# Kernel optimization log

Measured on AMD Instinct MI355X. Metric: run time of the kernel, lower is better.

## Reference

```python
import jax, jax.numpy as jnp
import numpy as np

NBINS = 256
HMIN, HMAX = 0.0, 255.0

def _histc(x, nbins=NBINS, lo=HMIN, hi=HMAX):
    # Faithful torch.histc: bin width (hi-lo)/nbins; values outside [lo,hi] ignored;
    # values == hi fall into the last bin. Returns float counts.
    xf = x.reshape(-1)
    width = (hi - lo) / nbins
    idx = jnp.floor((xf - lo) / width).astype(jnp.int32)
    idx = jnp.minimum(idx, nbins - 1)            # x == hi -> last bin
    in_range = (xf >= lo) & (xf <= hi)
    idx = jnp.where(in_range, idx, nbins)        # out-of-range -> dropped bucket
    hist = jnp.zeros(nbins + 1, dtype=x.dtype).at[idx].add(1.0)
    return hist[:nbins]

def setup_inputs() -> dict:
    key = jax.random.key(0)
    # intensity image with values in [0, 255]
    x = jax.random.uniform(key, (8192, 4096), dtype=jnp.float32) * 255.0
    return {"batchsize": 16, "input": x}

def reference(batchsize, input):
    hist = _histc(input)                          # [256] float counts
    # Original loop recomputes the same histc each iter and does
    # count += hist[0] (scalar broadcast into all 256 slots).
    count = jnp.zeros(NBINS, dtype=hist.dtype) + jnp.asarray(batchsize, hist.dtype) * hist[0]
    return (hist, count)
```

## Files before the change

kernel.cpp:

```cpp
#include <hip/hip_runtime.h>

#define NBINS 256
#define BLOCK 64
#define NQUAD 64
#define CNT_DW (NQUAD * 64)
#define LDS_DW (CNT_DW + 64)
#define BIN_SCALE (256.0f / 255.0f)
#define CAP_F4 62

__global__ void zero_out(float* __restrict__ out) {
    const int i = blockIdx.x * blockDim.x + threadIdx.x;
    if (i < 2 * NBINS) out[i] = 0.0f;
}

__device__ __forceinline__ void classify(float v, int t, int& dw, unsigned& inc) {
    int idx = (int)(v * BIN_SCALE);
    idx = idx < 255 ? idx : 255;
    const bool ok = (v >= 0.0f) && (v <= 255.0f);
    const int d = ((((unsigned)idx) >> 2) << 6) + t;
    dw = ok ? d : (CNT_DW + t);
    inc = 1u << ((idx & 3) << 3);
}

__global__ __launch_bounds__(BLOCK) void hist_kernel(const float* __restrict__ x,
                                                     unsigned int* __restrict__ partial,
                                                     float* __restrict__ out,
                                                     int n, int G, int use_ws) {
    __shared__ unsigned int cnt[LDS_DW];
    const int t = threadIdx.x;

    for (int i = t; i < LDS_DW; i += BLOCK) cnt[i] = 0u;
    __syncthreads();

    const int n4 = n >> 2;
    const float4* __restrict__ x4 = (const float4*)x;
    const int stride = G * BLOCK;
    int i = blockIdx.x * BLOCK + t;

    if (i < n4) {
        float4 v = x4[i];
        for (;;) {
            const int ni = i + stride;
            const bool more = ni < n4;
            float4 nv;
            if (more) nv = x4[ni];

            int d0, d1, d2, d3; unsigned s0, s1, s2, s3;
            classify(v.x, t, d0, s0);
            classify(v.y, t, d1, s1);
            classify(v.z, t, d2, s2);
            classify(v.w, t, d3, s3);

            unsigned o0 = cnt[d0], o1 = cnt[d1], o2 = cnt[d2], o3 = cnt[d3];
            cnt[d0] = o0 + s0;
            cnt[d1] = o1 + s1 + (d1 == d0 ? s0 : 0u);
            cnt[d2] = o2 + s2 + (d2 == d0 ? s0 : 0u) + (d2 == d1 ? s1 : 0u);
            cnt[d3] = o3 + s3 + (d3 == d0 ? s0 : 0u) + (d3 == d1 ? s1 : 0u)
                              + (d3 == d2 ? s2 : 0u);

            if (!more) break;
            v = nv; i = ni;
        }
    }
    for (int j = (n4 << 2) + blockIdx.x * BLOCK + t; j < n; j += stride) {
        int dw; unsigned inc;
        classify(x[j], t, dw, inc);
        cnt[dw] += inc;
    }
    __syncthreads();

    unsigned accA = 0, accB = 0;
#pragma unroll 16
    for (int k = 0; k < 64; ++k) {
        unsigned u = cnt[(t << 6) + ((t + k) & 63)];
        accA += u & 0x00FF00FFu;
        accB += (u >> 8) & 0x00FF00FFu;
    }
    const unsigned b0 = accA & 0xFFFFu, b2 = accA >> 16;
    const unsigned b1 = accB & 0xFFFFu, b3 = accB >> 16;

    if (use_ws) {
        ((uint4*)(partial + (size_t)blockIdx.x * NBINS))[t] = make_uint4(b0, b1, b2, b3);
    } else {
        if (b0) atomicAdd(&out[4 * t + 0], (float)b0);
        if (b1) atomicAdd(&out[4 * t + 1], (float)b1);
        if (b2) atomicAdd(&out[4 * t + 2], (float)b2);
        if (b3) atomicAdd(&out[4 * t + 3], (float)b3);
    }
}

__global__ __launch_bounds__(NBINS) void reduce_kernel(const unsigned int* __restrict__ partial,
                                                       float* __restrict__ out,
                                                       int G, int slice) {
    const int bin = threadIdx.x;
    const int g0 = blockIdx.x * slice;
    const int g1 = (g0 + slice < G) ? (g0 + slice) : G;
    unsigned s = 0;
    for (int g = g0; g < g1; ++g)
        s += partial[(size_t)g * NBINS + bin];
    if (s) atomicAdd(&out[bin], (float)s);
}

__global__ void count_kernel(const void* __restrict__ bs_raw,
                             float* __restrict__ out) {
    const int as_int = *(const int*)bs_raw;
    float bs;
    if (as_int >= 1 && as_int < (1 << 20)) {
        bs = (float)as_int;
    } else {
        bs = *(const float*)bs_raw;
    }
    out[NBINS + threadIdx.x] = bs * out[0];
}

extern "C" void kernel_launch(void* const* d_in, const int* in_sizes, int n_in,
                              void* d_out, int out_size, void* d_ws, size_t ws_size,
                              hipStream_t stream) {
    const void* bs_ptr;
    const float* x;
    int n;
    if (n_in >= 2 && in_sizes[0] == 1) {
        bs_ptr = d_in[0];
        x = (const float*)d_in[1];
        n = in_sizes[1];
    } else {
        bs_ptr = d_in[1];
        x = (const float*)d_in[0];
        n = in_sizes[0];
    }

    float* out = (float*)d_out;
    unsigned int* partial = (unsigned int*)d_ws;

    const long n4 = (long)n >> 2;
    int G = (int)((n4 + (long)BLOCK * CAP_F4 - 1) / ((long)BLOCK * CAP_F4));
    if (G < 1) G = 1;

    const size_t ws_need = (size_t)G * NBINS * sizeof(unsigned int);
    const int use_ws = (ws_size >= ws_need) ? 1 : 0;

    zero_out<<<2, 256, 0, stream>>>(out);
    hist_kernel<<<G, BLOCK, 0, stream>>>(x, partial, out, n, G, use_ws);
    if (use_ws) {
        const int slice = (G + NBINS - 1) / NBINS;
        reduce_kernel<<<NBINS, NBINS, 0, stream>>>(partial, out, G, slice);
    }
    count_kernel<<<1, NBINS, 0, stream>>>(bs_ptr, out);
}
```

Measured before the change: 216.6 us.

## Software-pipeline histogram loop with 4-deep load ring and deferred LDS writes

Replaces the single-prefetch grid-stride loop with a fixed-trip loop that keeps four float4 loads in flight in a register ring. The LDS read-modify-write is split across iterations: the next element's counters are read while the previous element's sums are written, to hide LDS latency. Out-of-range values now add zero to the thread's own slot instead of using a separate dump region, which shrinks LDS. Zeroing uses uint4 stores. This costs more registers and a more complex loop, and could limit occupancy.

```diff
diff --git a/kernel.cpp b/kernel.cpp
--- a/kernel.cpp
+++ b/kernel.cpp
@@ -2,9 +2,7 @@
 
 #define NBINS 256
 #define BLOCK 64
-#define NQUAD 64
-#define CNT_DW (NQUAD * 64)
-#define LDS_DW (CNT_DW + 64)
+#define CNT_DW (64 * 64)
 #define BIN_SCALE (256.0f / 255.0f)
 #define CAP_F4 62
 
@@ -17,33 +15,50 @@
     int idx = (int)(v * BIN_SCALE);
     idx = idx < 255 ? idx : 255;
     const bool ok = (v >= 0.0f) && (v <= 255.0f);
-    const int d = ((((unsigned)idx) >> 2) << 6) + t;
-    dw = ok ? d : (CNT_DW + t);
-    inc = 1u << ((idx & 3) << 3);
+    dw = ok ? (((((unsigned)idx) >> 2) << 6) + t) : t;
+    inc = ok ? (1u << ((idx & 3) << 3)) : 0u;
 }
 
 __global__ __launch_bounds__(BLOCK) void hist_kernel(const float* __restrict__ x,
                                                      unsigned int* __restrict__ partial,
                                                      float* __restrict__ out,
                                                      int n, int G, int use_ws) {
-    __shared__ unsigned int cnt[LDS_DW];
+    __shared__ unsigned int cnt[CNT_DW];
     const int t = threadIdx.x;
 
-    for (int i = t; i < LDS_DW; i += BLOCK) cnt[i] = 0u;
+    {
+        uint4* z4 = (uint4*)cnt;
+#pragma unroll
+        for (int i = 0; i < CNT_DW / 4 / BLOCK; ++i)
+            z4[t + i * BLOCK] = make_uint4(0u, 0u, 0u, 0u);
+    }
     __syncthreads();
 
     const int n4 = n >> 2;
     const float4* __restrict__ x4 = (const float4*)x;
-    const int stride = G * BLOCK;
-    int i = blockIdx.x * BLOCK + t;
+    const int S = G * BLOCK;
+    const int i0 = blockIdx.x * BLOCK + t;
+    const int K = n4 / S;
 
-    if (i < n4) {
-        float4 v = x4[i];
-        for (;;) {
-            const int ni = i + stride;
-            const bool more = ni < n4;
-            float4 nv;
-            if (more) nv = x4[ni];
+    if (K > 0) {
+        float4 ring[4];
+#pragma unroll
+        for (int d = 0; d < 4; ++d)
+            ring[d] = (d < K) ? x4[i0 + d * S] : make_float4(-1.f, -1.f, -1.f, -1.f);
+
+        float4 v = ring[0];
+        if (4 < K) ring[0] = x4[i0 + 4 * S];
+        int pd0, pd1, pd2, pd3; unsigned ps0, ps1, ps2, ps3;
+        classify(v.x, t, pd0, ps0);
+        classify(v.y, t, pd1, ps1);
+        classify(v.z, t, pd2, ps2);
+        classify(v.w, t, pd3, ps3);
+        unsigned po0 = cnt[pd0], po1 = cnt[pd1], po2 = cnt[pd2], po3 = cnt[pd3];
+
+#pragma unroll 4
+        for (int k = 1; k < K; ++k) {
+            v = ring[k & 3];
+            if (k + 4 < K) ring[k & 3] = x4[i0 + (k + 4) * S];
 
             int d0, d1, d2, d3; unsigned s0, s1, s2, s3;
             classify(v.x, t, d0, s0);
@@ -51,21 +66,40 @@
             classify(v.z, t, d2, s2);
             classify(v.w, t, d3, s3);
 
-            unsigned o0 = cnt[d0], o1 = cnt[d1], o2 = cnt[d2], o3 = cnt[d3];
-            cnt[d0] = o0 + s0;
-            cnt[d1] = o1 + s1 + (d1 == d0 ? s0 : 0u);
-            cnt[d2] = o2 + s2 + (d2 == d0 ? s0 : 0u) + (d2 == d1 ? s1 : 0u);
-            cnt[d3] = o3 + s3 + (d3 == d0 ? s0 : 0u) + (d3 == d1 ? s1 : 0u)
-                              + (d3 == d2 ? s2 : 0u);
+            unsigned w0 = po0 + ps0;
+            unsigned w1 = po1 + ps1 + (pd1 == pd0 ? ps0 : 0u);
+            unsigned w2 = po2 + ps2 + (pd2 == pd0 ? ps0 : 0u) + (pd2 == pd1 ? ps1 : 0u);
+            unsigned w3 = po3 + ps3 + (pd3 == pd0 ? ps0 : 0u) + (pd3 == pd1 ? ps1 : 0u)
+                                    + (pd3 == pd2 ? ps2 : 0u);
+            cnt[pd0] = w0; cnt[pd1] = w1; cnt[pd2] = w2; cnt[pd3] = w3;
 
-            if (!more) break;
-            v = nv; i = ni;
+            po0 = cnt[d0]; po1 = cnt[d1]; po2 = cnt[d2]; po3 = cnt[d3];
+            pd0 = d0; pd1 = d1; pd2 = d2; pd3 = d3;
+            ps0 = s0; ps1 = s1; ps2 = s2; ps3 = s3;
+        }
+        unsigned w0 = po0 + ps0;
+        unsigned w1 = po1 + ps1 + (pd1 == pd0 ? ps0 : 0u);
+        unsigned w2 = po2 + ps2 + (pd2 == pd0 ? ps0 : 0u) + (pd2 == pd1 ? ps1 : 0u);
+        unsigned w3 = po3 + ps3 + (pd3 == pd0 ? ps0 : 0u) + (pd3 == pd1 ? ps1 : 0u)
+                                + (pd3 == pd2 ? ps2 : 0u);
+        cnt[pd0] = w0; cnt[pd1] = w1; cnt[pd2] = w2; cnt[pd3] = w3;
+    }
+
+    {
+        const int it = i0 + K * S;
+        if (it < n4) {
+            float4 v = x4[it];
+            int d; unsigned s;
+            classify(v.x, t, d, s); cnt[d] += s;
+            classify(v.y, t, d, s); cnt[d] += s;
+            classify(v.z, t, d, s); cnt[d] += s;
+            classify(v.w, t, d, s); cnt[d] += s;
         }
     }
-    for (int j = (n4 << 2) + blockIdx.x * BLOCK + t; j < n; j += stride) {
-        int dw; unsigned inc;
-        classify(x[j], t, dw, inc);
-        cnt[dw] += inc;
+    for (int j = (n4 << 2) + i0; j < n; j += S) {
+        int d; unsigned s;
+        classify(x[j], t, d, s);
+        cnt[d] += s;
     }
     __syncthreads();
 
```

New measurement: 239.6 us. 10.6% more time.
